# Kernel tuning notes

Measured on AMD Instinct MI355X. Metric: run time of the kernel, lower is better.

The kernel has to match this reference:

```python
import jax, jax.numpy as jnp
import numpy as np
import math

NUM_HEADS = 16
HIDDEN = 1024
HEAD = HIDDEN // NUM_HEADS


def setup_inputs() -> dict:
    key = jax.random.key(0)
    ks = jax.random.split(key, 11)
    B, S, H = 2, 2048, HIDDEN
    s = 1.0 / math.sqrt(H)
    return {
        "q": jax.random.normal(ks[0], (B, S, H), jnp.float32),
        "k": jax.random.normal(ks[1], (B, S, H), jnp.float32),
        "v": jax.random.normal(ks[2], (B, S, H), jnp.float32),
        "Wq": jax.random.normal(ks[3], (H, H), jnp.float32) * s,
        "bq": jnp.zeros((H,), jnp.float32),
        "Wk": jax.random.normal(ks[4], (H, H), jnp.float32) * s,
        "bk": jnp.zeros((H,), jnp.float32),
        "Wv": jax.random.normal(ks[5], (H, H), jnp.float32) * s,
        "bv": jnp.zeros((H,), jnp.float32),
        "Wo": jax.random.normal(ks[6], (H, H), jnp.float32) * s,
        "bo": jnp.zeros((H,), jnp.float32),
    }


def reference(q, k, v, Wq, bq, Wk, bk, Wv, bv, Wo, bo):
    B, S, H = q.shape
    nh, hd = NUM_HEADS, HEAD
    # projections (torch Linear: x @ W.T + b)
    qp = (q @ Wq.T + bq).reshape(B, S, nh, hd).transpose(0, 2, 1, 3)  # [B,nh,S,hd]
    kp = (k @ Wk.T + bk).reshape(B, S, nh, hd).transpose(0, 2, 1, 3)
    vp = (v @ Wv.T + bv).reshape(B, S, nh, hd).transpose(0, 2, 1, 3)
    scores = jnp.einsum('bhqd,bhkd->bhqk', qp, kp) / math.sqrt(hd)
    attn = jax.nn.softmax(scores, axis=-1)  # [B,nh,S,S]
    o = jnp.einsum('bhqk,bhkd->bhqd', attn, vp)
    o = o.transpose(0, 2, 1, 3).reshape(B, S, H)
    return o @ Wo.T + bo
```

## Files before the change

kernel.cpp:

```cpp
#include <hip/hip_runtime.h>
#include <cstdint>
#include <type_traits>
#include <utility>

typedef __attribute__((ext_vector_type(8))) short short8;
typedef __attribute__((ext_vector_type(8))) __bf16 bf16x8_t;
typedef __attribute__((ext_vector_type(8))) _Float16 f16x8_t;
typedef __attribute__((ext_vector_type(4))) float f32x4;

template <typename V, typename = void>
struct mfma_takes : std::false_type {};
template <typename V>
struct mfma_takes<V, std::void_t<decltype(__builtin_amdgcn_mfma_f32_16x16x32_bf16(
    std::declval<V>(), std::declval<V>(), std::declval<f32x4>(), 0, 0, 0))>>
    : std::true_type {};

using frag_t = std::conditional_t<mfma_takes<bf16x8_t>::value, bf16x8_t, short8>;
static_assert(mfma_takes<bf16x8_t>::value || mfma_takes<short8>::value,
              "no usable mfma_f32_16x16x32_bf16 signature");

__device__ __forceinline__ f32x4 mfma16(frag_t a, frag_t b, f32x4 c) {
  return __builtin_amdgcn_mfma_f32_16x16x32_bf16(a, b, c, 0, 0, 0);
}

template <typename V, typename = void>
struct mfma_h_takes : std::false_type {};
template <typename V>
struct mfma_h_takes<V, std::void_t<decltype(__builtin_amdgcn_mfma_f32_16x16x32_f16(
    std::declval<V>(), std::declval<V>(), std::declval<f32x4>(), 0, 0, 0))>>
    : std::true_type {};

using hfrag_t = std::conditional_t<mfma_h_takes<f16x8_t>::value, f16x8_t, short8>;
static_assert(mfma_h_takes<f16x8_t>::value || mfma_h_takes<short8>::value,
              "no usable mfma_f32_16x16x32_f16 signature");

__device__ __forceinline__ f32x4 mfma16h(hfrag_t a, hfrag_t b, f32x4 c) {
  return __builtin_amdgcn_mfma_f32_16x16x32_f16(a, b, c, 0, 0, 0);
}

__device__ __forceinline__ void gld_lds16(const void* g, void* l) {
  __builtin_amdgcn_global_load_lds(
      (const __attribute__((address_space(1))) void*)(uintptr_t)g,
      (__attribute__((address_space(3))) void*)(uint32_t)(uintptr_t)l, 16, 0, 0);
}

__device__ __forceinline__ uint16_t bf16_rne(float x) {
  uint32_t u = __builtin_bit_cast(uint32_t, x);
  u += 0x7FFFu + ((u >> 16) & 1u);
  return (uint16_t)(u >> 16);
}
__device__ __forceinline__ float bf16_up(uint16_t h) {
  uint32_t u = ((uint32_t)h) << 16;
  return __builtin_bit_cast(float, u);
}
__device__ __forceinline__ void split2(float x, uint16_t& h, uint16_t& l) {
  h = bf16_rne(x);
  float r = x - bf16_up(h);
  l = bf16_rne(r);
}

__device__ __forceinline__ uint16_t f16_rne(float x) {
  return __builtin_bit_cast(uint16_t, (_Float16)x);
}
__device__ __forceinline__ float f16_up(uint16_t h) {
  return (float)__builtin_bit_cast(_Float16, h);
}

__device__ __forceinline__ float exp2_fast(float x) {
#if __has_builtin(__builtin_amdgcn_exp2f)
  return __builtin_amdgcn_exp2f(x);
#else
  return exp2f(x);
#endif
}
__device__ __forceinline__ uint32_t pk_f16(float a, float b) {
#if __has_builtin(__builtin_amdgcn_cvt_pkrtz)
  return __builtin_bit_cast(uint32_t, __builtin_amdgcn_cvt_pkrtz(a, b));
#else
  union { uint16_t u[2]; uint32_t w; } r;
  r.u[0] = f16_rne(a);
  r.u[1] = f16_rne(b);
  return r.w;
#endif
}

__device__ __forceinline__ int swz(int row, int col) {
  return row * 64 + ((((col >> 3) + row) & 7) << 3) + (col & 7);
}

struct SplitArgs {
  const float* src[4];
  uint16_t* hi[4];
  uint16_t* lo[4];
  int n4;
};
__global__ void split_multi(SplitArgs a) {
  const int z = blockIdx.y;
  int i = blockIdx.x * 256 + threadIdx.x;
  if (i >= a.n4) return;
  float4 x = ((const float4*)a.src[z])[i];
  ushort4 h, l;
  split2(x.x, h.x, l.x);
  split2(x.y, h.y, l.y);
  split2(x.z, h.z, l.z);
  split2(x.w, h.w, l.w);
  ((ushort4*)a.hi[z])[i] = h;
  if (a.lo[z]) ((ushort4*)a.lo[z])[i] = l;
}

struct QKVArgs {
  const uint16_t* Ah[3];
  const uint16_t* Al[3];
  const uint16_t* Bh[3];
  const float* bias[3];
  uint16_t* oH[3];
  uint16_t* oL[3];
};

__global__ __launch_bounds__(256, 3) void gemm_qkv(QKVArgs args) {
  __shared__ uint16_t lds[3][128][32];
  const int K = 1024;
  const int tid = threadIdx.x;
  const int wv = tid >> 6, lane = tid & 63;
  const int lm = lane & 15, g = lane >> 4;
  const int wm = (wv & 1) * 64, wn = (wv >> 1) * 64;
  const int z = blockIdx.z;
  const bool isT = (z == 2);
  const int t = blockIdx.x + 8 * blockIdx.y;
  const int kx = t & 7, j = t >> 3;
  const int sx = (j & 3) | ((kx & 1) << 2);
  const int sy = (j >> 2) | ((kx >> 1) << 3);
  const int gm0 = (isT ? sx : sy) * 128;
  const int gn0 = (isT ? sy : sx) * 128;

  const uint16_t* base[3] = {args.Ah[z] + (size_t)gm0 * K, args.Al[z] + (size_t)gm0 * K,
                             args.Bh[z] + (size_t)gn0 * K};
  const int rl = lane >> 2, cl = (lane & 3) * 8;

  f32x4 acc[4][4];
#pragma unroll
  for (int a = 0; a < 4; ++a)
#pragma unroll
    for (int b = 0; b < 4; ++b) acc[a][b] = (f32x4)0.0f;

#pragma unroll 1
  for (int kt = 0; kt < K; kt += 32) {
#pragma unroll
    for (int jj = 0; jj < 6; ++jj) {
      const int c = wv + 4 * jj;
      const int p = c >> 3, r16 = (c & 7) * 16;
      gld_lds16(base[p] + (size_t)(r16 + rl) * K + kt + cl, &lds[p][r16][0]);
    }
    __syncthreads();
    frag_t af[2][4];
#pragma unroll
    for (int mf = 0; mf < 4; ++mf) {
      af[0][mf] = *(const frag_t*)&lds[0][wm + mf * 16 + lm][g * 8];
      af[1][mf] = *(const frag_t*)&lds[1][wm + mf * 16 + lm][g * 8];
    }
#pragma unroll
    for (int nf = 0; nf < 4; ++nf) {
      frag_t bhf = *(const frag_t*)&lds[2][wn + nf * 16 + lm][g * 8];
#pragma unroll
      for (int mf = 0; mf < 4; ++mf) {
        acc[mf][nf] = mfma16(af[0][mf], bhf, acc[mf][nf]);
        acc[mf][nf] = mfma16(af[1][mf], bhf, acc[mf][nf]);
      }
    }
    __syncthreads();
  }
  const float* bias = args.bias[z];
  uint16_t* oH = args.oH[z];
  uint16_t* oL = args.oL[z];
#pragma unroll
  for (int mf = 0; mf < 4; ++mf) {
#pragma unroll
    for (int nf = 0; nf < 4; ++nf) {
      const int col = gn0 + wn + nf * 16 + lm;
#pragma unroll
      for (int i = 0; i < 4; ++i) {
        const int row = gm0 + wm + mf * 16 + g * 4 + i;
        float v = acc[mf][nf][i] + (isT ? bias[row] : bias[col]);
        uint16_t h = f16_rne(v);
        size_t addr;
        if (!isT) {
          addr = ((size_t)((row >> 11) * 16 + (col >> 6)) * 2048 + (row & 2047)) * 64 +
                 (col & 63);
        } else {
          addr = ((size_t)((col >> 11) * 1024 + row)) * 2048 + (col & 2047);
        }
        oH[addr] = h;
        if (oL) oL[addr] = f16_rne(v - f16_up(h));
      }
    }
  }
}

__global__ __launch_bounds__(256, 2) void gemm_o(
    const uint16_t* __restrict__ Ah, const uint16_t* __restrict__ Al,
    const uint16_t* __restrict__ Bh, const float* __restrict__ bias,
    float* __restrict__ out) {
  const int K = 1024, N = 1024;
  __shared__ uint16_t ldsA[2][64][32];
  __shared__ uint16_t ldsB[128][32];
  const int tid = threadIdx.x;
  const int wv = tid >> 6, lane = tid & 63;
  const int lm = lane & 15, g = lane >> 4;
  const int wm = (wv & 1) * 32, wn = (wv >> 1) * 64;
  const int t = blockIdx.x + 8 * blockIdx.y;
  const int kx = t & 7, j = t >> 3;
  const int sx = (j & 3) | ((kx & 1) << 2);
  const int sy = (j >> 2) | ((kx >> 1) << 4);
  const int gm0 = sy * 64, gn0 = sx * 128;
  const uint16_t* baseA[2] = {Ah + (size_t)gm0 * K, Al + (size_t)gm0 * K};
  const uint16_t* baseB = Bh + (size_t)gn0 * K;
  const int rl = lane >> 2, cl = (lane & 3) * 8;

  f32x4 acc[2][4];
#pragma unroll
  for (int a = 0; a < 2; ++a)
#pragma unroll
    for (int b = 0; b < 4; ++b) acc[a][b] = (f32x4)0.0f;

#pragma unroll 1
  for (int kt = 0; kt < K; kt += 32) {
#pragma unroll
    for (int jj = 0; jj < 4; ++jj) {
      const int c = wv + 4 * jj;
      if (c < 8) {
        const int p = c >> 2, r16 = (c & 3) * 16;
        gld_lds16(baseA[p] + (size_t)(r16 + rl) * K + kt + cl, &ldsA[p][r16][0]);
      } else {
        const int b = c - 8;
        gld_lds16(baseB + (size_t)(b * 16 + rl) * K + kt + cl, &ldsB[b * 16][0]);
      }
    }
    __syncthreads();
    frag_t af[2][2];
#pragma unroll
    for (int mf = 0; mf < 2; ++mf) {
      af[0][mf] = *(const frag_t*)&ldsA[0][wm + mf * 16 + lm][g * 8];
      af[1][mf] = *(const frag_t*)&ldsA[1][wm + mf * 16 + lm][g * 8];
    }
#pragma unroll
    for (int nf = 0; nf < 4; ++nf) {
      frag_t bhf = *(const frag_t*)&ldsB[wn + nf * 16 + lm][g * 8];
#pragma unroll
      for (int mf = 0; mf < 2; ++mf) {
        acc[mf][nf] = mfma16(af[0][mf], bhf, acc[mf][nf]);
        acc[mf][nf] = mfma16(af[1][mf], bhf, acc[mf][nf]);
      }
    }
    __syncthreads();
  }
#pragma unroll
  for (int mf = 0; mf < 2; ++mf)
#pragma unroll
    for (int nf = 0; nf < 4; ++nf) {
      const int col = gn0 + wn + nf * 16 + lm;
#pragma unroll
      for (int i = 0; i < 4; ++i) {
        const int row = gm0 + wm + mf * 16 + g * 4 + i;
        out[(size_t)row * N + col] = acc[mf][nf][i] + bias[col];
      }
    }
}

__global__ __launch_bounds__(256, 2) void attn_kernel(
    const uint16_t* __restrict__ Qh,
    const uint16_t* __restrict__ Kh,
    const uint16_t* __restrict__ Vh,
    float* __restrict__ opart, float* __restrict__ lpart) {
  __shared__ uint16_t kt[4096];
  __shared__ uint16_t vt[4096];
  __shared__ uint16_t pp[8192];
  const int tid = threadIdx.x;
  const int wave = tid >> 6, lane = tid & 63;
  const int lm = lane & 15, g = lane >> 4;
  const int linear = blockIdx.x + 32 * blockIdx.y;
  const int bh = (linear & 7) + 8 * (linear >> 8);
  const int qt = (linear >> 3) & 15;
  const int half = (linear >> 7) & 1;
  const int kvh = half * 1024;
  const size_t base = (size_t)bh * 131072;
  const int q0 = qt * 128 + wave * 32;

  hfrag_t qf[2][2];
#pragma unroll
  for (int b = 0; b < 2; ++b) {
    const size_t rb = base + (size_t)(q0 + b * 16 + lm) * 64 + g * 8;
    qf[b][0] = *(const hfrag_t*)(Qh + rb);
    qf[b][1] = *(const hfrag_t*)(Qh + rb + 32);
  }
  f32x4 oacc[2][4];
  f32x4 lacc[2];
#pragma unroll
  for (int mf = 0; mf < 2; ++mf) {
    lacc[mf] = (f32x4)0.0f;
#pragma unroll
    for (int nf = 0; nf < 4; ++nf) oacc[mf][nf] = (f32x4)0.0f;
  }
  short8 ones_s = (short8)(short)0x3C00;
  hfrag_t ones = __builtin_bit_cast(hfrag_t, ones_s);

  const int sr = tid >> 3;
  const int sc = (tid & 7) * 8;

  uint4 kr0, kr1, vr0, vr1;
  {
    const size_t ka = base + (size_t)(kvh + sr) * 64 + sc;
    kr0 = *(const uint4*)(Kh + ka);
    kr1 = *(const uint4*)(Kh + ka + 2048);
  }

  const float kExpScale = 0.12500000f * 1.44269504f;

#pragma unroll 1
  for (int it = 0; it < 16; ++it) {
    const int kv0 = kvh + it * 64;
    *(uint4*)&kt[swz(sr, sc)] = kr0;
    *(uint4*)&kt[swz(sr + 32, sc)] = kr1;
    __syncthreads();
    {
      const size_t va = base + (size_t)sr * 2048 + kv0 + sc;
      vr0 = *(const uint4*)(Vh + va);
      vr1 = *(const uint4*)(Vh + va + 65536);
    }
    f32x4 sct[4][2];
#pragma unroll
    for (int a = 0; a < 4; ++a)
#pragma unroll
      for (int b = 0; b < 2; ++b) sct[a][b] = (f32x4)0.0f;
    __builtin_amdgcn_s_setprio(1);
#pragma unroll
    for (int ks = 0; ks < 2; ++ks) {
#pragma unroll
      for (int a = 0; a < 4; ++a) {
        hfrag_t kfh = *(const hfrag_t*)&kt[swz(a * 16 + lm, ks * 32 + g * 8)];
#pragma unroll
        for (int b = 0; b < 2; ++b) {
          sct[a][b] = mfma16h(kfh, qf[b][ks], sct[a][b]);
        }
      }
    }
    __builtin_amdgcn_s_setprio(0);
#pragma unroll
    for (int a = 0; a < 4; ++a) {
#pragma unroll
      for (int b = 0; b < 2; ++b) {
        float e0 = exp2_fast(fminf(kExpScale * sct[a][b][0], 15.0f));
        float e1 = exp2_fast(fminf(kExpScale * sct[a][b][1], 15.0f));
        float e2 = exp2_fast(fminf(kExpScale * sct[a][b][2], 15.0f));
        float e3 = exp2_fast(fminf(kExpScale * sct[a][b][3], 15.0f));
        uint2 pk;
        pk.x = pk_f16(e0, e1);
        pk.y = pk_f16(e2, e3);
        *(uint2*)&pp[swz(wave * 32 + b * 16 + lm, a * 16 + g * 4)] = pk;
      }
    }
    *(uint4*)&vt[swz(sr, sc)] = vr0;
    *(uint4*)&vt[swz(sr + 32, sc)] = vr1;
    __syncthreads();
    if (it + 1 < 16) {
      const size_t ka = base + (size_t)(kv0 + 64 + sr) * 64 + sc;
      kr0 = *(const uint4*)(Kh + ka);
      kr1 = *(const uint4*)(Kh + ka + 2048);
    }
    __builtin_amdgcn_s_setprio(1);
#pragma unroll
    for (int ks = 0; ks < 2; ++ks) {
      hfrag_t pa[2];
#pragma unroll
      for (int mf = 0; mf < 2; ++mf) {
        pa[mf] = *(const hfrag_t*)&pp[swz(wave * 32 + mf * 16 + lm, ks * 32 + g * 8)];
        lacc[mf] = mfma16h(pa[mf], ones, lacc[mf]);
      }
#pragma unroll
      for (int nf = 0; nf < 4; ++nf) {
        hfrag_t vbh = *(const hfrag_t*)&vt[swz(nf * 16 + lm, ks * 32 + g * 8)];
#pragma unroll
        for (int mf = 0; mf < 2; ++mf) {
          oacc[mf][nf] = mfma16h(pa[mf], vbh, oacc[mf][nf]);
        }
      }
    }
    __builtin_amdgcn_s_setprio(0);
  }
  const int obase = (half * 32 + bh) * 2048;
#pragma unroll
  for (int mf = 0; mf < 2; ++mf) {
#pragma unroll
    for (int i = 0; i < 4; ++i) {
      const int qrow = qt * 128 + wave * 32 + mf * 16 + g * 4 + i;
      float* orow = opart + ((size_t)obase + qrow) * 64;
#pragma unroll
      for (int nf = 0; nf < 4; ++nf) orow[nf * 16 + lm] = oacc[mf][nf][i];
      if (lm == 0) lpart[obase + qrow] = lacc[mf][i];
    }
  }
}

__global__ void combine_kernel(const float* __restrict__ opart,
                               const float* __restrict__ lpart,
                               uint16_t* __restrict__ oh, uint16_t* __restrict__ ol) {
  const int idx = blockIdx.x * 256 + threadIdx.x;
  const float4 a = ((const float4*)opart)[idx];
  const float4 b = ((const float4*)(opart + 4194304))[idx];
  const int row = idx >> 4;
  const float linv = 1.0f / (lpart[row] + lpart[65536 + row]);
  const int bh = row >> 11, qq = row & 2047;
  const int bb = bh >> 4, hh = bh & 15;
  const size_t o = ((size_t)(bb * 2048 + qq)) * 1024 + hh * 64 + (idx & 15) * 4;
  ushort4 H, L;
  float v;
  v = (a.x + b.x) * linv; split2(v, H.x, L.x);
  v = (a.y + b.y) * linv; split2(v, H.y, L.y);
  v = (a.z + b.z) * linv; split2(v, H.z, L.z);
  v = (a.w + b.w) * linv; split2(v, H.w, L.w);
  *(ushort4*)(oh + o) = H;
  *(ushort4*)(ol + o) = L;
}

extern "C" void kernel_launch(void* const* d_in, const int* in_sizes, int n_in,
                              void* d_out, int out_size, void* d_ws, size_t ws_size,
                              hipStream_t stream) {
  const float* q = (const float*)d_in[0];
  const float* k = (const float*)d_in[1];
  const float* v = (const float*)d_in[2];
  const float* Wq = (const float*)d_in[3];
  const float* bq = (const float*)d_in[4];
  const float* Wk = (const float*)d_in[5];
  const float* bk = (const float*)d_in[6];
  const float* Wv = (const float*)d_in[7];
  const float* bv = (const float*)d_in[8];
  const float* Wo = (const float*)d_in[9];
  const float* bo = (const float*)d_in[10];

  const size_t NX = 4194304;
  const size_t NW = 1048576;
  uint16_t* p = (uint16_t*)d_ws;
  uint16_t* xqh = p; p += NX; uint16_t* xql = p; p += NX;
  uint16_t* xkh = p; p += NX; uint16_t* xkl = p; p += NX;
  uint16_t* xvh = p; p += NX; uint16_t* xvl = p; p += NX;
  uint16_t* wqh = p; p += NW; uint16_t* wql = p; p += NW;
  uint16_t* wkh = p; p += NW; uint16_t* wkl = p; p += NW;
  uint16_t* wvh = p; p += NW; uint16_t* wvl = p; p += NW;
  uint16_t* woh = p; p += NW; uint16_t* wol = p; p += NW;
  uint16_t* qph = p; p += NX; uint16_t* qpl = p; p += NX;
  uint16_t* kph = p; p += NX; uint16_t* kpl = p; p += NX;
  uint16_t* vth = p; p += NX; uint16_t* vtl = p; p += NX;
  uint16_t* oh = xqh;
  uint16_t* ol = xql;
  float* opart = (float*)xkh;
  float* lpart = opart + 2 * 4194304;

  SplitArgs sx;
  sx.src[0] = q;  sx.hi[0] = xqh; sx.lo[0] = xql;
  sx.src[1] = k;  sx.hi[1] = xkh; sx.lo[1] = xkl;
  sx.src[2] = v;  sx.hi[2] = xvh; sx.lo[2] = nullptr;
  sx.src[3] = nullptr; sx.hi[3] = nullptr; sx.lo[3] = nullptr;
  sx.n4 = (int)(NX / 4);
  split_multi<<<dim3((unsigned)(NX / 4 / 256), 3), 256, 0, stream>>>(sx);

  SplitArgs sw;
  sw.src[0] = Wq; sw.hi[0] = wqh; sw.lo[0] = nullptr;
  sw.src[1] = Wk; sw.hi[1] = wkh; sw.lo[1] = nullptr;
  sw.src[2] = Wv; sw.hi[2] = wvh; sw.lo[2] = wvl;
  sw.src[3] = Wo; sw.hi[3] = woh; sw.lo[3] = nullptr;
  sw.n4 = (int)(NW / 4);
  split_multi<<<dim3((unsigned)(NW / 4 / 256), 4), 256, 0, stream>>>(sw);

  QKVArgs qa;
  qa.Ah[0] = xqh; qa.Al[0] = xql; qa.Bh[0] = wqh;
  qa.bias[0] = bq; qa.oH[0] = qph; qa.oL[0] = nullptr;
  qa.Ah[1] = xkh; qa.Al[1] = xkl; qa.Bh[1] = wkh;
  qa.bias[1] = bk; qa.oH[1] = kph; qa.oL[1] = nullptr;
  qa.Ah[2] = wvh; qa.Al[2] = wvl; qa.Bh[2] = xvh;
  qa.bias[2] = bv; qa.oH[2] = vth; qa.oL[2] = nullptr;
  gemm_qkv<<<dim3(8, 32, 3), 256, 0, stream>>>(qa);

  attn_kernel<<<dim3(32, 32), 256, 0, stream>>>(qph, kph, vth, opart, lpart);
  combine_kernel<<<4096, 256, 0, stream>>>(opart, lpart, oh, ol);

  gemm_o<<<dim3(8, 64), 256, 0, stream>>>(oh, ol, woh, bo, (float*)d_out);
}
```

Baseline: 264.7 us.

## Switch projection GEMMs from split bf16 hi/lo to single fp16 with swizzled LDS

Replaces the two-term bf16 hi/lo split of the activations and weights with a single fp16 conversion in the QKV and output projection GEMMs. This halves the MFMA count and the global/LDS traffic for the A operand, and drops the lo buffers and their writes in the split and combine kernels. It also adds an XOR-style column swizzle on the global-to-LDS loads and the fragment reads to reduce LDS bank conflicts. The cost is lower precision, since fp16 has an 11-bit mantissa against the roughly 16 effective bits of bf16 hi+lo, and fp16 range limits apply.

```diff
diff --git a/kernel.cpp b/kernel.cpp
--- a/kernel.cpp
+++ b/kernel.cpp
@@ -4,24 +4,8 @@
 #include <utility>
 
 typedef __attribute__((ext_vector_type(8))) short short8;
-typedef __attribute__((ext_vector_type(8))) __bf16 bf16x8_t;
 typedef __attribute__((ext_vector_type(8))) _Float16 f16x8_t;
 typedef __attribute__((ext_vector_type(4))) float f32x4;
-
-template <typename V, typename = void>
-struct mfma_takes : std::false_type {};
-template <typename V>
-struct mfma_takes<V, std::void_t<decltype(__builtin_amdgcn_mfma_f32_16x16x32_bf16(
-    std::declval<V>(), std::declval<V>(), std::declval<f32x4>(), 0, 0, 0))>>
-    : std::true_type {};
-
-using frag_t = std::conditional_t<mfma_takes<bf16x8_t>::value, bf16x8_t, short8>;
-static_assert(mfma_takes<bf16x8_t>::value || mfma_takes<short8>::value,
-              "no usable mfma_f32_16x16x32_bf16 signature");
-
-__device__ __forceinline__ f32x4 mfma16(frag_t a, frag_t b, f32x4 c) {
-  return __builtin_amdgcn_mfma_f32_16x16x32_bf16(a, b, c, 0, 0, 0);
-}
 
 template <typename V, typename = void>
 struct mfma_h_takes : std::false_type {};
@@ -42,21 +26,6 @@
   __builtin_amdgcn_global_load_lds(
       (const __attribute__((address_space(1))) void*)(uintptr_t)g,
       (__attribute__((address_space(3))) void*)(uint32_t)(uintptr_t)l, 16, 0, 0);
-}
-
-__device__ __forceinline__ uint16_t bf16_rne(float x) {
-  uint32_t u = __builtin_bit_cast(uint32_t, x);
-  u += 0x7FFFu + ((u >> 16) & 1u);
-  return (uint16_t)(u >> 16);
-}
-__device__ __forceinline__ float bf16_up(uint16_t h) {
-  uint32_t u = ((uint32_t)h) << 16;
-  return __builtin_bit_cast(float, u);
-}
-__device__ __forceinline__ void split2(float x, uint16_t& h, uint16_t& l) {
-  h = bf16_rne(x);
-  float r = x - bf16_up(h);
-  l = bf16_rne(r);
 }
 
 __device__ __forceinline__ uint16_t f16_rne(float x) {
@@ -99,18 +68,24 @@
   int i = blockIdx.x * 256 + threadIdx.x;
   if (i >= a.n4) return;
   float4 x = ((const float4*)a.src[z])[i];
-  ushort4 h, l;
-  split2(x.x, h.x, l.x);
-  split2(x.y, h.y, l.y);
-  split2(x.z, h.z, l.z);
-  split2(x.w, h.w, l.w);
+  ushort4 h;
+  h.x = f16_rne(x.x);
+  h.y = f16_rne(x.y);
+  h.z = f16_rne(x.z);
+  h.w = f16_rne(x.w);
   ((ushort4*)a.hi[z])[i] = h;
-  if (a.lo[z]) ((ushort4*)a.lo[z])[i] = l;
+  if (a.lo[z]) {
+    ushort4 l;
+    l.x = f16_rne(x.x - f16_up(h.x));
+    l.y = f16_rne(x.y - f16_up(h.y));
+    l.z = f16_rne(x.z - f16_up(h.z));
+    l.w = f16_rne(x.w - f16_up(h.w));
+    ((ushort4*)a.lo[z])[i] = l;
+  }
 }
 
 struct QKVArgs {
   const uint16_t* Ah[3];
-  const uint16_t* Al[3];
   const uint16_t* Bh[3];
   const float* bias[3];
   uint16_t* oH[3];
@@ -118,7 +93,7 @@
 };
 
 __global__ __launch_bounds__(256, 3) void gemm_qkv(QKVArgs args) {
-  __shared__ uint16_t lds[3][128][32];
+  __shared__ uint16_t lds[2][128][32];
   const int K = 1024;
   const int tid = threadIdx.x;
   const int wv = tid >> 6, lane = tid & 63;
@@ -133,9 +108,11 @@
   const int gm0 = (isT ? sx : sy) * 128;
   const int gn0 = (isT ? sy : sx) * 128;
 
-  const uint16_t* base[3] = {args.Ah[z] + (size_t)gm0 * K, args.Al[z] + (size_t)gm0 * K,
+  const uint16_t* base[2] = {args.Ah[z] + (size_t)gm0 * K,
                              args.Bh[z] + (size_t)gn0 * K};
-  const int rl = lane >> 2, cl = (lane & 3) * 8;
+  const int rl = lane >> 2;
+  const int scl = (((lane & 3) - (rl >> 1)) & 3) * 8;
+  const int ucol = ((g + (lm >> 1)) & 3) * 8;
 
   f32x4 acc[4][4];
 #pragma unroll
@@ -146,25 +123,23 @@
 #pragma unroll 1
   for (int kt = 0; kt < K; kt += 32) {
 #pragma unroll
-    for (int jj = 0; jj < 6; ++jj) {
+    for (int jj = 0; jj < 4; ++jj) {
       const int c = wv + 4 * jj;
       const int p = c >> 3, r16 = (c & 7) * 16;
-      gld_lds16(base[p] + (size_t)(r16 + rl) * K + kt + cl, &lds[p][r16][0]);
-    }
-    __syncthreads();
-    frag_t af[2][4];
+      gld_lds16(base[p] + (size_t)(r16 + rl) * K + kt + scl, &lds[p][r16][0]);
+    }
+    __syncthreads();
+    hfrag_t af[4];
 #pragma unroll
     for (int mf = 0; mf < 4; ++mf) {
-      af[0][mf] = *(const frag_t*)&lds[0][wm + mf * 16 + lm][g * 8];
-      af[1][mf] = *(const frag_t*)&lds[1][wm + mf * 16 + lm][g * 8];
+      af[mf] = *(const hfrag_t*)&lds[0][wm + mf * 16 + lm][ucol];
     }
 #pragma unroll
     for (int nf = 0; nf < 4; ++nf) {
-      frag_t bhf = *(const frag_t*)&lds[2][wn + nf * 16 + lm][g * 8];
+      hfrag_t bhf = *(const hfrag_t*)&lds[1][wn + nf * 16 + lm][ucol];
 #pragma unroll
       for (int mf = 0; mf < 4; ++mf) {
-        acc[mf][nf] = mfma16(af[0][mf], bhf, acc[mf][nf]);
-        acc[mf][nf] = mfma16(af[1][mf], bhf, acc[mf][nf]);
+        acc[mf][nf] = mfma16h(af[mf], bhf, acc[mf][nf]);
       }
     }
     __syncthreads();
@@ -197,11 +172,10 @@
 }
 
 __global__ __launch_bounds__(256, 2) void gemm_o(
-    const uint16_t* __restrict__ Ah, const uint16_t* __restrict__ Al,
-    const uint16_t* __restrict__ Bh, const float* __restrict__ bias,
-    float* __restrict__ out) {
+    const uint16_t* __restrict__ Ah, const uint16_t* __restrict__ Bh,
+    const float* __restrict__ bias, float* __restrict__ out) {
   const int K = 1024, N = 1024;
-  __shared__ uint16_t ldsA[2][64][32];
+  __shared__ uint16_t ldsA[64][32];
   __shared__ uint16_t ldsB[128][32];
   const int tid = threadIdx.x;
   const int wv = tid >> 6, lane = tid & 63;
@@ -212,9 +186,11 @@
   const int sx = (j & 3) | ((kx & 1) << 2);
   const int sy = (j >> 2) | ((kx >> 1) << 4);
   const int gm0 = sy * 64, gn0 = sx * 128;
-  const uint16_t* baseA[2] = {Ah + (size_t)gm0 * K, Al + (size_t)gm0 * K};
+  const uint16_t* baseA = Ah + (size_t)gm0 * K;
   const uint16_t* baseB = Bh + (size_t)gn0 * K;
-  const int rl = lane >> 2, cl = (lane & 3) * 8;
+  const int rl = lane >> 2;
+  const int scl = (((lane & 3) - (rl >> 1)) & 3) * 8;
+  const int ucol = ((g + (lm >> 1)) & 3) * 8;
 
   f32x4 acc[2][4];
 #pragma unroll
@@ -225,30 +201,27 @@
 #pragma unroll 1
   for (int kt = 0; kt < K; kt += 32) {
 #pragma unroll
-    for (int jj = 0; jj < 4; ++jj) {
+    for (int jj = 0; jj < 3; ++jj) {
       const int c = wv + 4 * jj;
-      if (c < 8) {
-        const int p = c >> 2, r16 = (c & 3) * 16;
-        gld_lds16(baseA[p] + (size_t)(r16 + rl) * K + kt + cl, &ldsA[p][r16][0]);
+      if (c < 4) {
+        gld_lds16(baseA + (size_t)(c * 16 + rl) * K + kt + scl, &ldsA[c * 16][0]);
       } else {
-        const int b = c - 8;
-        gld_lds16(baseB + (size_t)(b * 16 + rl) * K + kt + cl, &ldsB[b * 16][0]);
-      }
-    }
-    __syncthreads();
-    frag_t af[2][2];
+        const int b = c - 4;
+        gld_lds16(baseB + (size_t)(b * 16 + rl) * K + kt + scl, &ldsB[b * 16][0]);
+      }
+    }
+    __syncthreads();
+    hfrag_t af[2];
 #pragma unroll
     for (int mf = 0; mf < 2; ++mf) {
-      af[0][mf] = *(const frag_t*)&ldsA[0][wm + mf * 16 + lm][g * 8];
-      af[1][mf] = *(const frag_t*)&ldsA[1][wm + mf * 16 + lm][g * 8];
+      af[mf] = *(const hfrag_t*)&ldsA[wm + mf * 16 + lm][ucol];
     }
 #pragma unroll
     for (int nf = 0; nf < 4; ++nf) {
-      frag_t bhf = *(const frag_t*)&ldsB[wn + nf * 16 + lm][g * 8];
+      hfrag_t bhf = *(const hfrag_t*)&ldsB[wn + nf * 16 + lm][ucol];
 #pragma unroll
       for (int mf = 0; mf < 2; ++mf) {
-        acc[mf][nf] = mfma16(af[0][mf], bhf, acc[mf][nf]);
-        acc[mf][nf] = mfma16(af[1][mf], bhf, acc[mf][nf]);
+        acc[mf][nf] = mfma16h(af[mf], bhf, acc[mf][nf]);
       }
     }
     __syncthreads();
@@ -402,7 +375,7 @@
 
 __global__ void combine_kernel(const float* __restrict__ opart,
                                const float* __restrict__ lpart,
-                               uint16_t* __restrict__ oh, uint16_t* __restrict__ ol) {
+                               uint16_t* __restrict__ oh) {
   const int idx = blockIdx.x * 256 + threadIdx.x;
   const float4 a = ((const float4*)opart)[idx];
   const float4 b = ((const float4*)(opart + 4194304))[idx];
@@ -411,14 +384,12 @@
   const int bh = row >> 11, qq = row & 2047;
   const int bb = bh >> 4, hh = bh & 15;
   const size_t o = ((size_t)(bb * 2048 + qq)) * 1024 + hh * 64 + (idx & 15) * 4;
-  ushort4 H, L;
-  float v;
-  v = (a.x + b.x) * linv; split2(v, H.x, L.x);
-  v = (a.y + b.y) * linv; split2(v, H.y, L.y);
-  v = (a.z + b.z) * linv; split2(v, H.z, L.z);
-  v = (a.w + b.w) * linv; split2(v, H.w, L.w);
+  ushort4 H;
+  H.x = f16_rne((a.x + b.x) * linv);
+  H.y = f16_rne((a.y + b.y) * linv);
+  H.z = f16_rne((a.z + b.z) * linv);
+  H.w = f16_rne((a.w + b.w) * linv);
   *(ushort4*)(oh + o) = H;
-  *(ushort4*)(ol + o) = L;
 }
 
 extern "C" void kernel_launch(void* const* d_in, const int* in_sizes, int n_in,
@@ -450,13 +421,12 @@
   uint16_t* kph = p; p += NX; uint16_t* kpl = p; p += NX;
   uint16_t* vth = p; p += NX; uint16_t* vtl = p; p += NX;
   uint16_t* oh = xqh;
-  uint16_t* ol = xql;
   float* opart = (float*)xkh;
   float* lpart = opart + 2 * 4194304;
 
   SplitArgs sx;
-  sx.src[0] = q;  sx.hi[0] = xqh; sx.lo[0] = xql;
-  sx.src[1] = k;  sx.hi[1] = xkh; sx.lo[1] = xkl;
+  sx.src[0] = q;  sx.hi[0] = xqh; sx.lo[0] = nullptr;
+  sx.src[1] = k;  sx.hi[1] = xkh; sx.lo[1] = nullptr;
   sx.src[2] = v;  sx.hi[2] = xvh; sx.lo[2] = nullptr;
   sx.src[3] = nullptr; sx.hi[3] = nullptr; sx.lo[3] = nullptr;
   sx.n4 = (int)(NX / 4);
@@ -465,22 +435,19 @@
   SplitArgs sw;
   sw.src[0] = Wq; sw.hi[0] = wqh; sw.lo[0] = nullptr;
   sw.src[1] = Wk; sw.hi[1] = wkh; sw.lo[1] = nullptr;
-  sw.src[2] = Wv; sw.hi[2] = wvh; sw.lo[2] = wvl;
+  sw.src[2] = Wv; sw.hi[2] = wvh; sw.lo[2] = nullptr;
   sw.src[3] = Wo; sw.hi[3] = woh; sw.lo[3] = nullptr;
   sw.n4 = (int)(NW / 4);
   split_multi<<<dim3((unsigned)(NW / 4 / 256), 4), 256, 0, stream>>>(sw);
 
   QKVArgs qa;
-  qa.Ah[0] = xqh; qa.Al[0] = xql; qa.Bh[0] = wqh;
-  qa.bias[0] = bq; qa.oH[0] = qph; qa.oL[0] = nullptr;
-  qa.Ah[1] = xkh; qa.Al[1] = xkl; qa.Bh[1] = wkh;
-  qa.bias[1] = bk; qa.oH[1] = kph; qa.oL[1] = nullptr;
-  qa.Ah[2] = wvh; qa.Al[2] = wvl; qa.Bh[2] = xvh;
-  qa.bias[2] = bv; qa.oH[2] = vth; qa.oL[2] = nullptr;
+  qa.Ah[0] = xqh; qa.Bh[0] = wqh; qa.bias[0] = bq; qa.oH[0] = qph; qa.oL[0] = nullptr;
+  qa.Ah[1] = xkh; qa.Bh[1] = wkh; qa.bias[1] = bk; qa.oH[1] = kph; qa.oL[1] = nullptr;
+  qa.Ah[2] = wvh; qa.Bh[2] = xvh; qa.bias[2] = bv; qa.oH[2] = vth; qa.oL[2] = nullptr;
   gemm_qkv<<<dim3(8, 32, 3), 256, 0, stream>>>(qa);
 
   attn_kernel<<<dim3(32, 32), 256, 0, stream>>>(qph, kph, vth, opart, lpart);
-  combine_kernel<<<4096, 256, 0, stream>>>(opart, lpart, oh, ol);
-
-  gemm_o<<<dim3(8, 64), 256, 0, stream>>>(oh, ol, woh, bo, (float*)d_out);
-}
+  combine_kernel<<<4096, 256, 0, stream>>>(opart, lpart, oh);
+
+  gemm_o<<<dim3(8, 64), 256, 0, stream>>>(oh, woh, bo, (float*)d_out);
+}
```

New measurement: 239.5 us. 9.5% less time.
